# Kernel optimization log

Hardware: AMD Instinct MI355X
Metric: run time of the kernel (lower is better)

Reference implementation:

```python
import jax, jax.numpy as jnp
import numpy as np

B, N, S, K = 16, 4, 64, 50        # batch, n_answers, q_len, n_boxes
VD, QD, H = 1024, 768, 512        # v_dim, q_dim, num_hid


def setup_inputs() -> dict:
    key = jax.random.key(0)
    ks = jax.random.split(key, 10)
    inp = {
        "v": jax.random.normal(ks[0], (B, 1, K, VD), dtype=jnp.float32),
        "q": jax.random.normal(ks[1], (B, N, S, 1, QD), dtype=jnp.float32),
        "box_mask": jax.random.randint(ks[2], (B, K), 0, 2, dtype=jnp.int32),
        "tags_attention": jax.random.normal(ks[3], (B, K), dtype=jnp.float32),
        # learned params (nn.Linear stores weight as [out, in])
        "Wv": jax.random.normal(ks[4], (H, VD), dtype=jnp.float32) * 0.02,
        "bv": jnp.zeros((H,), dtype=jnp.float32),
        "Wq": jax.random.normal(ks[5], (H, QD), dtype=jnp.float32) * 0.02,
        "bq": jnp.zeros((H,), dtype=jnp.float32),
        "Wl": jax.random.normal(ks[6], (1, H), dtype=jnp.float32) * 0.02,
        "bl": jnp.zeros((1,), dtype=jnp.float32),
    }
    return inp


def reference(v, q, box_mask, tags_attention, Wv, bv, Wq, bq, Wl, bl):
    # v_proj = Linear(v).unsqueeze(1): [B,1,K,H] -> [B,1,1,K,H]
    v_proj = (jnp.einsum('bokd,hd->bokh', v, Wv) + bv)[:, None]
    # q_proj: [B,N,S,1,H]
    q_proj = jnp.einsum('bnsod,hd->bnsoh', q, Wq) + bq
    # broadcast add + tanh: joint_repr [B,N,S,K,H] (the big intermediate)
    joint_repr = jnp.tanh(v_proj + q_proj)
    # score reduce over H: logits [B,N,S,K]
    logits = jnp.einsum('bnskh,oh->bnsko', joint_repr, Wl)[..., 0] + bl[0]
    # masked softmax over boxes with mask box_mask[:,None,None] -> [B,1,1,K]
    mask = (box_mask > 0)[:, None, None]
    w = jax.nn.softmax(jnp.where(mask, logits, jnp.float32(-1e9)), axis=-1)
    return w
```

## Files before the change

### kernel.cpp

```cpp
#include <hip/hip_runtime.h>
#include <hip/hip_bf16.h>
#include <cstddef>


typedef __attribute__((ext_vector_type(2))) float          f32x2;
typedef __attribute__((ext_vector_type(4))) float          f32x4;
typedef __attribute__((ext_vector_type(8))) short          bfrag;
typedef __attribute__((ext_vector_type(2))) unsigned int   u32x2;
typedef __attribute__((ext_vector_type(4))) unsigned int   u32x4;
typedef __attribute__((ext_vector_type(4))) unsigned short u16x4;

#define SBAR   __builtin_amdgcn_s_barrier()
#define SCHED0 __builtin_amdgcn_sched_barrier(0)

__device__ __forceinline__ void gload16(const void* g, void* l) {
  __builtin_amdgcn_global_load_lds((const __attribute__((address_space(1))) void*)g,
                                   (__attribute__((address_space(3))) void*)l, 16, 0, 0);
}

__device__ __forceinline__ unsigned int cvtpk(float a, float b) {
  unsigned int r;
  asm("v_cvt_pk_bf16_f32 %0, %1, %2" : "=v"(r) : "v"(a), "v"(b));
  return r;
}

__device__ __forceinline__ float bf2f(unsigned short u) {
  return __uint_as_float((unsigned int)u << 16);
}

template<int CTRL>
__device__ __forceinline__ float dpp_add(float x) {
  int r = __builtin_amdgcn_update_dpp(0, __float_as_int(x), CTRL, 0xF, 0xF, false);
  return x + __int_as_float(r);
}

__global__ void __launch_bounds__(256) cvt_all(
    const float* __restrict__ v, const float* __restrict__ wv,
    const float* __restrict__ q, const float* __restrict__ wq,
    unsigned short* __restrict__ vb, unsigned short* __restrict__ wvb,
    unsigned short* __restrict__ qb, unsigned short* __restrict__ wqb) {
  const int total = 610304;
  for (int f = blockIdx.x * 256 + threadIdx.x; f < total; f += gridDim.x * 256) {
    const float* src; unsigned short* dst; int off;
    if (f < 102400)       { src = v;  dst = vb;  off = f; }
    else if (f < 167936)  { src = wv; dst = wvb; off = f - 102400; }
    else if (f < 561152)  { src = q;  dst = qb;  off = f - 167936; }
    else                  { src = wq; dst = wqb; off = f - 561152; }
    f32x4 x0 = ((const f32x4*)src)[off * 2];
    f32x4 x1 = ((const f32x4*)src)[off * 2 + 1];
    u32x4 p;
    p[0] = cvtpk(x0[0], x0[1]); p[1] = cvtpk(x0[2], x0[3]);
    p[2] = cvtpk(x1[0], x1[1]); p[3] = cvtpk(x1[2], x1[3]);
    ((u32x4*)dst)[off] = p;
  }
}

__global__ void __launch_bounds__(256) gemm_bf16(
    const unsigned short* __restrict__ vb, const unsigned short* __restrict__ qb,
    const unsigned short* __restrict__ wvb, const unsigned short* __restrict__ wqb,
    const float* __restrict__ bv, const float* __restrict__ bq,
    unsigned short* __restrict__ evw, unsigned short* __restrict__ qpw) {
  __shared__ unsigned short As[2][64 * 64];
  __shared__ unsigned short Bs[2][64 * 64];

  const int id = blockIdx.x;
  const int m  = (id & 7) + ((id >> 6) << 3);
  const int nt = (id >> 3) & 7;
  if (m >= 77) return;

  const int t = threadIdx.x;

  const unsigned short* A; const unsigned short* W; const float* bias;
  int M, Kd, m0;
  const bool vpath = (m < 13);
  if (vpath) { A = vb; W = wvb; bias = bv; M = 800;  Kd = 1024; m0 = m * 64; }
  else       { A = qb; W = wqb; bias = bq; M = 4096; Kd = 768;  m0 = (m - 13) * 64; }
  const int n0 = nt * 64;

  const int lane = t & 63;
  const int wave = t >> 6;
  const int wm   = wave >> 1;
  const int wn   = wave & 1;
  const int la   = lane & 15;
  const int lb   = lane >> 4;

  const int row1 = t >> 3;
  const int p1   = (t & 7) ^ (row1 & 7);
  int grA1 = m0 + row1;      if (grA1 >= M) grA1 = M - 1;
  int grA2 = m0 + row1 + 32; if (grA2 >= M) grA2 = M - 1;
  const unsigned short* srcA1 = A + (size_t)grA1 * Kd + p1 * 8;
  const unsigned short* srcA2 = A + (size_t)grA2 * Kd + p1 * 8;
  const unsigned short* srcB1 = W + (size_t)(n0 + row1) * Kd + p1 * 8;
  const unsigned short* srcB2 = W + (size_t)(n0 + row1 + 32) * Kd + p1 * 8;

  const int d1 = wave * 512;
  const int d2 = 2048 + wave * 512;

  auto STAGE = [&](int buf, int s) {
    const int o = s * 64;
    gload16(srcA1 + o, &As[buf][d1]);
    gload16(srcA2 + o, &As[buf][d2]);
    gload16(srcB1 + o, &Bs[buf][d1]);
    gload16(srcB2 + o, &Bs[buf][d2]);
  };

  f32x4 acc[2][2] = {};

  auto compute = [&](const unsigned short* sa, const unsigned short* sb) {
    bfrag af[2][2], bf[2][2];
#pragma unroll
    for (int r = 0; r < 2; ++r)
#pragma unroll
      for (int kk = 0; kk < 2; ++kk) {
        int rowa = wm * 32 + r * 16 + la;
        af[r][kk] = *(const bfrag*)((const char*)sa +
                     ((rowa * 128 + kk * 64 + lb * 16) ^ ((rowa & 7) << 4)));
        int rowb = wn * 32 + r * 16 + la;
        bf[r][kk] = *(const bfrag*)((const char*)sb +
                     ((rowb * 128 + kk * 64 + lb * 16) ^ ((rowb & 7) << 4)));
      }
#pragma unroll
    for (int kk = 0; kk < 2; ++kk)
#pragma unroll
      for (int r = 0; r < 2; ++r)
#pragma unroll
        for (int c = 0; c < 2; ++c)
          acc[r][c] = __builtin_amdgcn_mfma_f32_16x16x32_bf16(af[r][kk], bf[c][kk], acc[r][c], 0, 0, 0);
  };

  const int nsteps = Kd >> 6;
  STAGE(0, 0);
  STAGE(1, 1);
  for (int s = 0; s < nsteps; ++s) {
    if (s + 1 < nsteps) { asm volatile("s_waitcnt vmcnt(4)" ::: "memory"); }
    else                { asm volatile("s_waitcnt vmcnt(0)" ::: "memory"); }
    SCHED0;
    SBAR; SCHED0;
    compute(As[s & 1], Bs[s & 1]);
    SBAR; SCHED0;
    if (s + 2 < nsteps) STAGE(s & 1, s + 2);
  }

  const float CEXP = 2.885390081777927f;
  unsigned short* C = vpath ? evw : qpw;
#pragma unroll
  for (int c = 0; c < 2; ++c) {
    int col = n0 + wn * 32 + c * 16 + la;
    float bcol = bias[col];
#pragma unroll
    for (int r = 0; r < 2; ++r) {
      int mbase = m0 + wm * 32 + r * 16 + lb * 4;
#pragma unroll
      for (int e = 0; e < 4; ++e) {
        int mr = mbase + e;
        if (mr < M) {
          float val = __builtin_amdgcn_exp2f((acc[r][c][e] + bcol) * CEXP);
          C[(size_t)mr * 512 + col] = (unsigned short)cvtpk(val, val);
        }
      }
    }
  }
}

__global__ void
__attribute__((amdgpu_flat_work_group_size(512, 512), amdgpu_waves_per_eu(4, 4)))
stage3_kernel(
    const unsigned short* __restrict__ ev, const unsigned short* __restrict__ qp,
    const float* __restrict__ wl, const int* __restrict__ box_mask,
    float* __restrict__ out) {
  __shared__ unsigned short vpS[50][512];
  __shared__ float redS[8][64][8];

  const int b    = blockIdx.y;
  const int grp  = blockIdx.x;
  const int t    = threadIdx.x;
  const int wv   = t >> 6;
  const int lane = t & 63;
  const int row0 = b * 256 + grp * 16 + wv * 2;

  const unsigned short* q0 = qp + (size_t)row0 * 512;
  float eq0[8], eq1[8], wlr[8];
#pragma unroll
  for (int j = 0; j < 2; ++j) {
    u16x4 a = *(const u16x4*)&q0[j * 256 + 4 * lane];
    u16x4 c = *(const u16x4*)&q0[512 + j * 256 + 4 * lane];
    f32x4 w = *(const f32x4*)&wl[j * 256 + 4 * lane];
#pragma unroll
    for (int e = 0; e < 4; ++e) {
      eq0[j * 4 + e] = bf2f(a[e]);
      eq1[j * 4 + e] = bf2f(c[e]);
      wlr[j * 4 + e] = -2.f * w[e];
    }
  }

  {
    const unsigned short* src = ev + (size_t)b * 25600 + lane * 8;
#pragma unroll
    for (int i = 0; i < 7; ++i) {
      int kr = i * 8 + wv;
      if (kr < 50) gload16(src + kr * 512, &vpS[kr][0]);
    }
  }
  __syncthreads();

  const int g  = lane >> 4;
  const int li = lane & 15;

#pragma unroll 1
  for (int kc = 0; kc < 5; ++kc) {
    float a0[10], a1[10];
#pragma unroll
    for (int i = 0; i < 10; ++i) { a0[i] = 0.f; a1[i] = 0.f; }

#pragma unroll
    for (int i = 0; i < 10; ++i) {
      const unsigned short* vr = &vpS[kc * 10 + i][0];
      u16x4 va  = *(const u16x4*)&vr[4 * lane];
      u16x4 vb2 = *(const u16x4*)&vr[256 + 4 * lane];
#pragma unroll
      for (int e = 0; e < 4; ++e) {
        float evf = bf2f(va[e]);
        a0[i] = fmaf(wlr[e], __builtin_amdgcn_rcpf(fmaf(evf, eq0[e], 1.f)), a0[i]);
        a1[i] = fmaf(wlr[e], __builtin_amdgcn_rcpf(fmaf(evf, eq1[e], 1.f)), a1[i]);
      }
#pragma unroll
      for (int e = 0; e < 4; ++e) {
        float evf = bf2f(vb2[e]);
        a0[i] = fmaf(wlr[4 + e], __builtin_amdgcn_rcpf(fmaf(evf, eq0[4 + e], 1.f)), a0[i]);
        a1[i] = fmaf(wlr[4 + e], __builtin_amdgcn_rcpf(fmaf(evf, eq1[4 + e], 1.f)), a1[i]);
      }
    }

#pragma unroll
    for (int i = 0; i < 10; ++i) {
      int k = kc * 10 + i;
      float s0 = a0[i], s1 = a1[i];
      s0 = dpp_add<0x128>(s0); s0 = dpp_add<0x124>(s0);
      s0 = dpp_add<0x122>(s0); s0 = dpp_add<0x121>(s0);
      s1 = dpp_add<0x128>(s1); s1 = dpp_add<0x124>(s1);
      s1 = dpp_add<0x122>(s1); s1 = dpp_add<0x121>(s1);
      if (li == (k & 15)) {
        f32x2 p; p[0] = s0; p[1] = s1;
        *(f32x2*)&redS[wv][k][g * 2] = p;
      }
    }
  }

  const int k = lane;
  f32x4 ra = *(const f32x4*)&redS[wv][k][0];
  f32x4 rb = *(const f32x4*)&redS[wv][k][4];
  float l0 = (ra[0] + ra[2]) + (rb[0] + rb[2]);
  float l1 = (ra[1] + ra[3]) + (rb[1] + rb[3]);

  int   msk = (k < 50) ? box_mask[b * 50 + k] : 0;
  bool  on  = (k < 50 && msk > 0);
  float L0 = on ? l0 : -1e9f;
  float L1 = on ? l1 : -1e9f;

  float m0 = L0, m1 = L1;
#pragma unroll
  for (int off = 32; off; off >>= 1) {
    m0 = fmaxf(m0, __shfl_xor(m0, off));
    m1 = fmaxf(m1, __shfl_xor(m1, off));
  }
  const float LOG2E = 1.4426950408889634f;
  float e0 = (k < 50) ? __builtin_amdgcn_exp2f((L0 - m0) * LOG2E) : 0.f;
  float e1 = (k < 50) ? __builtin_amdgcn_exp2f((L1 - m1) * LOG2E) : 0.f;
  float s0 = e0, s1 = e1;
#pragma unroll
  for (int off = 32; off; off >>= 1) {
    s0 += __shfl_xor(s0, off);
    s1 += __shfl_xor(s1, off);
  }

  if (k < 50) {
    out[(size_t)row0 * 50 + k]       = e0 / s0;
    out[(size_t)(row0 + 1) * 50 + k] = e1 / s1;
  }
}

extern "C" void kernel_launch(void* const* d_in, const int* in_sizes, int n_in,
                              void* d_out, int out_size, void* d_ws, size_t ws_size,
                              hipStream_t stream) {
  const float* v        = (const float*)d_in[0];
  const float* q        = (const float*)d_in[1];
  const int*   box_mask = (const int*)d_in[2];
  const float* Wv       = (const float*)d_in[4];
  const float* bv       = (const float*)d_in[5];
  const float* Wq       = (const float*)d_in[6];
  const float* bq       = (const float*)d_in[7];
  const float* Wl       = (const float*)d_in[8];
  float* out = (float*)d_out;

  char* ws = (char*)d_ws;
  unsigned short* qpw = (unsigned short*)(ws);
  unsigned short* evw = (unsigned short*)(ws + 4194304);
  unsigned short* vb  = (unsigned short*)(ws + 5013504);
  unsigned short* qb  = (unsigned short*)(ws + 6651904);
  unsigned short* wvb = (unsigned short*)(ws + 12943360);
  unsigned short* wqb = (unsigned short*)(ws + 13991936);

  cvt_all<<<2048, 256, 0, stream>>>(v, Wv, q, Wq, vb, wvb, qb, wqb);
  gemm_bf16<<<dim3(640), 256, 0, stream>>>(vb, qb, wvb, wqb, bv, bq, evw, qpw);
  stage3_kernel<<<dim3(16, 16), 512, 0, stream>>>(evw, qpw, Wl, box_mask, out);
}
```

Before: 44.74 us.

## Fuse fp32-to-bf16 activation conversion into GEMM A-tile staging

The separate conversion pass over v and q is dropped. The GEMM now reads fp32 activations straight into registers, packs them to bf16 and writes them into swizzled LDS. Only the weights still go through a small conversion kernel. This saves a full write and read of about 6 MB of bf16 activations, at the cost of a register-staged A path with a hand-unrolled double-buffer schedule. Each GEMM block also rereads its fp32 A rows once per N-tile, which is more global traffic per block.

```diff
diff --git a/kernel.cpp b/kernel.cpp
--- a/kernel.cpp
+++ b/kernel.cpp
@@ -6,7 +6,6 @@
 typedef __attribute__((ext_vector_type(2))) float          f32x2;
 typedef __attribute__((ext_vector_type(4))) float          f32x4;
 typedef __attribute__((ext_vector_type(8))) short          bfrag;
-typedef __attribute__((ext_vector_type(2))) unsigned int   u32x2;
 typedef __attribute__((ext_vector_type(4))) unsigned int   u32x4;
 typedef __attribute__((ext_vector_type(4))) unsigned short u16x4;
 
@@ -34,18 +33,14 @@
   return x + __int_as_float(r);
 }
 
-__global__ void __launch_bounds__(256) cvt_all(
-    const float* __restrict__ v, const float* __restrict__ wv,
-    const float* __restrict__ q, const float* __restrict__ wq,
-    unsigned short* __restrict__ vb, unsigned short* __restrict__ wvb,
-    unsigned short* __restrict__ qb, unsigned short* __restrict__ wqb) {
-  const int total = 610304;
+__global__ void __launch_bounds__(256) cvt_w(
+    const float* __restrict__ wv, const float* __restrict__ wq,
+    unsigned short* __restrict__ wvb, unsigned short* __restrict__ wqb) {
+  const int total = 114688;
   for (int f = blockIdx.x * 256 + threadIdx.x; f < total; f += gridDim.x * 256) {
     const float* src; unsigned short* dst; int off;
-    if (f < 102400)       { src = v;  dst = vb;  off = f; }
-    else if (f < 167936)  { src = wv; dst = wvb; off = f - 102400; }
-    else if (f < 561152)  { src = q;  dst = qb;  off = f - 167936; }
-    else                  { src = wq; dst = wqb; off = f - 561152; }
+    if (f < 65536) { src = wv; dst = wvb; off = f; }
+    else           { src = wq; dst = wqb; off = f - 65536; }
     f32x4 x0 = ((const f32x4*)src)[off * 2];
     f32x4 x1 = ((const f32x4*)src)[off * 2 + 1];
     u32x4 p;
@@ -56,7 +51,7 @@
 }
 
 __global__ void __launch_bounds__(256) gemm_bf16(
-    const unsigned short* __restrict__ vb, const unsigned short* __restrict__ qb,
+    const float* __restrict__ vA, const float* __restrict__ qA,
     const unsigned short* __restrict__ wvb, const unsigned short* __restrict__ wqb,
     const float* __restrict__ bv, const float* __restrict__ bq,
     unsigned short* __restrict__ evw, unsigned short* __restrict__ qpw) {
@@ -70,11 +65,11 @@
 
   const int t = threadIdx.x;
 
-  const unsigned short* A; const unsigned short* W; const float* bias;
+  const float* A; const unsigned short* W; const float* bias;
   int M, Kd, m0;
   const bool vpath = (m < 13);
-  if (vpath) { A = vb; W = wvb; bias = bv; M = 800;  Kd = 1024; m0 = m * 64; }
-  else       { A = qb; W = wqb; bias = bq; M = 4096; Kd = 768;  m0 = (m - 13) * 64; }
+  if (vpath) { A = vA; W = wvb; bias = bv; M = 800;  Kd = 1024; m0 = m * 64; }
+  else       { A = qA; W = wqb; bias = bq; M = 4096; Kd = 768;  m0 = (m - 13) * 64; }
   const int n0 = nt * 64;
 
   const int lane = t & 63;
@@ -84,22 +79,41 @@
   const int la   = lane & 15;
   const int lb   = lane >> 4;
 
+  const int srow = t >> 2;
+  const int skq  = (t & 3) * 16;
+  int grA = m0 + srow; if (grA >= M) grA = M - 1;
+  const float* ArowF = A + (size_t)grA * Kd + skq;
+
+  const int o0 = (srow * 128 + skq * 2)      ^ ((srow & 7) << 4);
+  const int o1 = (srow * 128 + skq * 2 + 16) ^ ((srow & 7) << 4);
+
+  f32x4 rA[4], rB[4];
+
+  auto loadA = [&](f32x4* r, int s) {
+    const float* ap = ArowF + s * 64;
+#pragma unroll
+    for (int i = 0; i < 4; ++i) r[i] = *(const f32x4*)&ap[i * 4];
+  };
+
+  auto writeA = [&](unsigned short* dst, const f32x4* r) {
+    u32x4 p;
+    p[0] = cvtpk(r[0][0], r[0][1]); p[1] = cvtpk(r[0][2], r[0][3]);
+    p[2] = cvtpk(r[1][0], r[1][1]); p[3] = cvtpk(r[1][2], r[1][3]);
+    *(u32x4*)((char*)dst + o0) = p;
+    p[0] = cvtpk(r[2][0], r[2][1]); p[1] = cvtpk(r[2][2], r[2][3]);
+    p[2] = cvtpk(r[3][0], r[3][1]); p[3] = cvtpk(r[3][2], r[3][3]);
+    *(u32x4*)((char*)dst + o1) = p;
+  };
+
   const int row1 = t >> 3;
   const int p1   = (t & 7) ^ (row1 & 7);
-  int grA1 = m0 + row1;      if (grA1 >= M) grA1 = M - 1;
-  int grA2 = m0 + row1 + 32; if (grA2 >= M) grA2 = M - 1;
-  const unsigned short* srcA1 = A + (size_t)grA1 * Kd + p1 * 8;
-  const unsigned short* srcA2 = A + (size_t)grA2 * Kd + p1 * 8;
   const unsigned short* srcB1 = W + (size_t)(n0 + row1) * Kd + p1 * 8;
   const unsigned short* srcB2 = W + (size_t)(n0 + row1 + 32) * Kd + p1 * 8;
-
   const int d1 = wave * 512;
   const int d2 = 2048 + wave * 512;
 
-  auto STAGE = [&](int buf, int s) {
+  auto STAGE_B = [&](int buf, int s) {
     const int o = s * 64;
-    gload16(srcA1 + o, &As[buf][d1]);
-    gload16(srcA2 + o, &As[buf][d2]);
     gload16(srcB1 + o, &Bs[buf][d1]);
     gload16(srcB2 + o, &Bs[buf][d2]);
   };
@@ -129,16 +143,42 @@
   };
 
   const int nsteps = Kd >> 6;
-  STAGE(0, 0);
-  STAGE(1, 1);
-  for (int s = 0; s < nsteps; ++s) {
-    if (s + 1 < nsteps) { asm volatile("s_waitcnt vmcnt(4)" ::: "memory"); }
-    else                { asm volatile("s_waitcnt vmcnt(0)" ::: "memory"); }
-    SCHED0;
+  loadA(rA, 0);
+  STAGE_B(0, 0);
+  loadA(rB, 1);
+  STAGE_B(1, 1);
+  writeA(As[0], rA);
+  asm volatile("s_waitcnt vmcnt(6)" ::: "memory"); SCHED0;
+  asm volatile("s_waitcnt lgkmcnt(0)" ::: "memory"); SCHED0;
+  SBAR; SCHED0;
+  for (int s = 0; ; s += 2) {
+    compute(As[0], Bs[0]);
     SBAR; SCHED0;
-    compute(As[s & 1], Bs[s & 1]);
+    {
+      const bool h2 = (s + 2 < nsteps);
+      if (h2) loadA(rA, s + 2);
+      writeA(As[1], rB);
+      if (h2) STAGE_B(0, s + 2);
+      if (h2) { asm volatile("s_waitcnt vmcnt(6)" ::: "memory"); }
+      else    { asm volatile("s_waitcnt vmcnt(0)" ::: "memory"); }
+      SCHED0;
+      asm volatile("s_waitcnt lgkmcnt(0)" ::: "memory"); SCHED0;
+      SBAR; SCHED0;
+    }
+    compute(As[1], Bs[1]);
+    if (s + 2 >= nsteps) break;
     SBAR; SCHED0;
-    if (s + 2 < nsteps) STAGE(s & 1, s + 2);
+    {
+      const bool h3 = (s + 3 < nsteps);
+      if (h3) loadA(rB, s + 3);
+      writeA(As[0], rA);
+      if (h3) STAGE_B(1, s + 3);
+      if (h3) { asm volatile("s_waitcnt vmcnt(6)" ::: "memory"); }
+      else    { asm volatile("s_waitcnt vmcnt(0)" ::: "memory"); }
+      SCHED0;
+      asm volatile("s_waitcnt lgkmcnt(0)" ::: "memory"); SCHED0;
+      SBAR; SCHED0;
+    }
   }
 
   const float CEXP = 2.885390081777927f;
@@ -295,12 +335,10 @@
   char* ws = (char*)d_ws;
   unsigned short* qpw = (unsigned short*)(ws);
   unsigned short* evw = (unsigned short*)(ws + 4194304);
-  unsigned short* vb  = (unsigned short*)(ws + 5013504);
-  unsigned short* qb  = (unsigned short*)(ws + 6651904);
-  unsigned short* wvb = (unsigned short*)(ws + 12943360);
-  unsigned short* wqb = (unsigned short*)(ws + 13991936);
-
-  cvt_all<<<2048, 256, 0, stream>>>(v, Wv, q, Wq, vb, wvb, qb, wqb);
-  gemm_bf16<<<dim3(640), 256, 0, stream>>>(vb, qb, wvb, wqb, bv, bq, evw, qpw);
+  unsigned short* wvb = (unsigned short*)(ws + 5013504);
+  unsigned short* wqb = (unsigned short*)(ws + 6062080);
+
+  cvt_w<<<448, 256, 0, stream>>>(Wv, Wq, wvb, wqb);
+  gemm_bf16<<<dim3(640), 256, 0, stream>>>(v, q, wvb, wqb, bv, bq, evw, qpw);
   stage3_kernel<<<dim3(16, 16), 512, 0, stream>>>(evw, qpw, Wl, box_mask, out);
 }
```

New measurement: 48.76 us. 9.0% more time.
